# Optimization experiments

Hardware: AMD Instinct MI355X
Metric: run time of the kernel (lower is better)

## Reference

```python
import jax, jax.numpy as jnp
import numpy as np

HIDDEN = 4096
N_HEADS = 32
N_KV_HEADS = 8
HEAD_DIM = 128
ROPE_BASE = 10000.0


def setup_inputs() -> dict:
    key = jax.random.key(0)
    k1, k2, k3, k4, k5 = jax.random.split(key, 5)
    s = 0.02  # init scale for weights
    return {
        "hidden_states": jax.random.normal(k1, (1, 2048, HIDDEN), dtype=jnp.float32),
        "Wq": jax.random.normal(k2, (N_HEADS * HEAD_DIM, HIDDEN), dtype=jnp.float32) * s,
        "Wk": jax.random.normal(k3, (N_KV_HEADS * HEAD_DIM, HIDDEN), dtype=jnp.float32) * s,
        "Wv": jax.random.normal(k4, (N_KV_HEADS * HEAD_DIM, HIDDEN), dtype=jnp.float32) * s,
        "Wo": jax.random.normal(k5, (HIDDEN, HIDDEN), dtype=jnp.float32) * s,
    }


def _rope(x, cos, sin):
    # x: [B, H, T, D]; cos/sin: [T, D/2] -> rotate split halves (Llama style)
    d2 = x.shape[-1] // 2
    x1, x2 = x[..., :d2], x[..., d2:]
    return jnp.concatenate([x1 * cos - x2 * sin, x1 * sin + x2 * cos], axis=-1)


def reference(hidden_states, Wq, Wk, Wv, Wo):
    B, T, _ = hidden_states.shape
    H, Hkv, D = N_HEADS, N_KV_HEADS, HEAD_DIM
    G = H // Hkv  # kv groups

    q = jnp.einsum("bth,qh->btq", hidden_states, Wq).reshape(B, T, H, D).transpose(0, 2, 1, 3)
    k = jnp.einsum("bth,kh->btk", hidden_states, Wk).reshape(B, T, Hkv, D).transpose(0, 2, 1, 3)
    v = jnp.einsum("bth,vh->btv", hidden_states, Wv).reshape(B, T, Hkv, D).transpose(0, 2, 1, 3)

    # RoPE (position_offset = 0)
    positions = jnp.arange(T, dtype=jnp.float32)
    inv_freq = ROPE_BASE ** (-jnp.arange(0, D, 2, dtype=jnp.float32) / D)  # [D/2]
    angles = positions[:, None] * inv_freq[None, :]                        # [T, D/2]
    cos, sin = jnp.cos(angles), jnp.sin(angles)
    q = _rope(q, cos, sin)
    k = _rope(k, cos, sin)

    # GQA attention without materializing expanded K/V: group query heads
    qg = q.reshape(B, Hkv, G, T, D)
    scale = 1.0 / jnp.sqrt(jnp.asarray(D, dtype=q.dtype))
    scores = jnp.einsum("bkgtd,bksd->bkgts", qg, k) * scale  # [B, Hkv, G, T, T]
    causal = jnp.tril(jnp.ones((T, T), dtype=bool))
    scores = jnp.where(causal, scores, jnp.finfo(scores.dtype).min)
    probs = jax.nn.softmax(scores, axis=-1)
    attn = jnp.einsum("bkgts,bksd->bkgtd", probs, v)          # [B, Hkv, G, T, D]
    attn = attn.reshape(B, H, T, D).transpose(0, 2, 1, 3).reshape(B, T, H * D)

    return jnp.einsum("btq,oq->bto", attn, Wo)
```

## Files before the change

kernel.cpp:

```cpp
#include <hip/hip_runtime.h>
#include <stdint.h>

#define T_SEQ   2048
#define HID     4096
#define NH      32
#define NKV     8
#define HD      128
#define QCOLS   6144
#define QK_SCALE 0.08838834764831845f

typedef _Float16 half_t;
typedef _Float16 half8 __attribute__((ext_vector_type(8)));
typedef _Float16 half4v __attribute__((ext_vector_type(4)));
typedef float    f32x4 __attribute__((ext_vector_type(4)));

typedef __attribute__((address_space(1))) const void cg_void;
typedef __attribute__((address_space(3))) void lds_void;

__global__ __launch_bounds__(256) void cast_all_k(const float* __restrict__ X,
                                                  const float* __restrict__ Wq,
                                                  const float* __restrict__ Wk,
                                                  const float* __restrict__ Wv,
                                                  const float* __restrict__ Wo,
                                                  half_t* __restrict__ Xh,
                                                  half_t* __restrict__ Wqkvh,
                                                  half_t* __restrict__ Woh) {
  int i = blockIdx.x * 256 + threadIdx.x;
  const float* src; half_t* dst; int off;
  if (i < 2097152)      { src = X;  dst = Xh;               off = i; }
  else if (i < 6291456) { src = Wq; dst = Wqkvh;            off = i - 2097152; }
  else if (i < 7340032) { src = Wk; dst = Wqkvh + 16777216; off = i - 6291456; }
  else if (i < 8388608) { src = Wv; dst = Wqkvh + 20971520; off = i - 7340032; }
  else                  { src = Wo; dst = Woh;              off = i - 8388608; }
  f32x4 v = *(const f32x4*)(src + (size_t)off * 4);
  half4v o;
  o[0] = (half_t)v[0]; o[1] = (half_t)v[1]; o[2] = (half_t)v[2]; o[3] = (half_t)v[3];
  *(half4v*)(dst + (size_t)off * 4) = o;
}

__global__ __launch_bounds__(256) void rope_tables_k(float* __restrict__ cs) {
  int idx = blockIdx.x * 256 + threadIdx.x;
  int t = idx >> 6, i = idx & 63;
  float inv = expf(-(float)i * 0.14391156831212787f);
  float a = (float)t * inv;
  cs[idx] = cosf(a);
  cs[131072 + idx] = sinf(a);
}

__global__ __launch_bounds__(256) void rope_apply_k(half_t* __restrict__ QKV,
                                                    const float* __restrict__ cs) {
  int idx = blockIdx.x * 256 + threadIdx.x;
  int i = idx & 63;
  int rem = idx >> 6;
  int head = rem % 40;
  int t = rem / 40;
  int colbase = (head < 32) ? head * HD : HID + (head - 32) * HD;
  size_t base = (size_t)t * QCOLS + colbase;
  float c = cs[t * 64 + i], s = cs[131072 + t * 64 + i];
  float x1 = (float)QKV[base + i];
  float x2 = (float)QKV[base + 64 + i];
  float o1 = x1 * c - x2 * s;
  float o2 = x1 * s + x2 * c;
  if (head < 32) { o1 *= QK_SCALE; o2 *= QK_SCALE; }
  QKV[base + i]      = (half_t)o1;
  QKV[base + 64 + i] = (half_t)o2;
}

__global__ __launch_bounds__(256) void transpose_v_k(const half_t* __restrict__ QKV,
                                                     half_t* __restrict__ Vt) {
  int idx = blockIdx.x * 256 + threadIdx.x;
  int d  = idx & 127;
  int ts = (idx >> 7) & 255;
  int kh = idx >> 15;
  half8 o;
#pragma unroll
  for (int i = 0; i < 8; ++i)
    o[i] = QKV[(size_t)(ts * 8 + i) * QCOLS + HID + NKV * HD + kh * HD + d];
  *(half8*)&Vt[(size_t)kh * (HD * T_SEQ) + (size_t)d * T_SEQ + ts * 8] = o;
}

template <int BM, int BN, int OUT_HALF>
__global__ __launch_bounds__(512, 2) void gemm8p_k(const half_t* __restrict__ A,
                                                   const half_t* __restrict__ Bm,
                                                   void* __restrict__ Cout,
                                                   int M, int N, int K) {
  constexpr int MF = BM / 32;
  constexpr int NF = BN / 64;
  constexpr int MH = MF / 2;
  constexpr int LA = BM / 64;
  constexpr int LB = BN / 64;
  __shared__ half_t Al[2][BM * 64];
  __shared__ half_t Bl[2][BN * 64];

  const int nbm = M / BM;
  const int nwg = nbm * (N / BN);
  const int bid = blockIdx.x;
  const int swz = (bid & 7) * (nwg >> 3) + (bid >> 3);
  const int brow = (swz % nbm) * BM;
  const int bcol = (swz / nbm) * BN;
  const int tid = threadIdx.x;
  const int lane = tid & 63, wid = tid >> 6;
  const int wr = wid >> 2, wc = wid & 3;
  const int lr = lane & 15, hi = lane >> 4;
  const int wrow = wr * (MF * 16), wcol = wc * (NF * 16);

  const half_t* Ab = A + (size_t)brow * K;
  const half_t* Bb = Bm + (size_t)bcol * K;

  f32x4 acc[MF][NF] = {};
  half8 afr[MH], bfr[NF];

#define STAGE_A(l, k0, buf) { \
    int c_ = (l) * 512 + tid; int r_ = c_ >> 3, s_ = c_ & 7; \
    __builtin_amdgcn_global_load_lds( \
      (cg_void*)(Ab + (size_t)r_ * K + (k0) + ((s_ ^ (r_ & 7)) * 8)), \
      (lds_void*)(&Al[buf][((l) * 512 + wid * 64) * 8]), 16, 0, 0); }
#define STAGE_B(l, k0, buf) { \
    int c_ = (l) * 512 + tid; int r_ = c_ >> 3, s_ = c_ & 7; \
    __builtin_amdgcn_global_load_lds( \
      (cg_void*)(Bb + (size_t)r_ * K + (k0) + ((s_ ^ (r_ & 7)) * 8)), \
      (lds_void*)(&Bl[buf][((l) * 512 + wid * 64) * 8]), 16, 0, 0); }
#define RD_A(i, mh, kk, buf) { \
    int row_ = wrow + ((mh) * MH + (i)) * 16 + lr; int ks_ = (kk) * 4 + hi; \
    afr[i] = *(const half8*)&Al[buf][row_ * 64 + ((ks_ ^ (row_ & 7)) * 8)]; }
#define RD_B(n, kk, buf) { \
    int row_ = wcol + (n) * 16 + lr; int ks_ = (kk) * 4 + hi; \
    bfr[n] = *(const half8*)&Bl[buf][row_ * 64 + ((ks_ ^ (row_ & 7)) * 8)]; }
#define MFMA_PH(mh) { \
    __builtin_amdgcn_s_setprio(1); \
    _Pragma("unroll") for (int i_ = 0; i_ < MH; ++i_) \
      _Pragma("unroll") for (int n_ = 0; n_ < NF; ++n_) \
        acc[(mh) * MH + i_][n_] = __builtin_amdgcn_mfma_f32_16x16x32_f16( \
            afr[i_], bfr[n_], acc[(mh) * MH + i_][n_], 0, 0, 0); \
    __builtin_amdgcn_s_setprio(0); }

#define DO_TILE(T, BUF) { \
    const int kn_ = ((T) + 1) * 64; const bool pf_ = ((T) + 1) < NT; \
     \
    if (pf_) { _Pragma("unroll") for (int l_ = 0; l_ < LA; ++l_) STAGE_A(l_, kn_, (BUF) ^ 1); } \
    _Pragma("unroll") for (int n_ = 0; n_ < NF; ++n_) RD_B(n_, 0, BUF); \
    _Pragma("unroll") for (int i_ = 0; i_ < MH; ++i_) RD_A(i_, 0, 0, BUF); \
    MFMA_PH(0); \
    __builtin_amdgcn_s_barrier(); __builtin_amdgcn_sched_barrier(0); \
     \
    if (pf_) { _Pragma("unroll") for (int l_ = 0; l_ < LB; ++l_) STAGE_B(l_, kn_, (BUF) ^ 1); } \
    _Pragma("unroll") for (int i_ = 0; i_ < MH; ++i_) RD_A(i_, 1, 0, BUF); \
    MFMA_PH(1); \
    __builtin_amdgcn_s_barrier(); __builtin_amdgcn_sched_barrier(0); \
     \
    _Pragma("unroll") for (int n_ = 0; n_ < NF; ++n_) RD_B(n_, 1, BUF); \
    _Pragma("unroll") for (int i_ = 0; i_ < MH; ++i_) RD_A(i_, 1, 1, BUF); \
    MFMA_PH(1); \
    __builtin_amdgcn_s_barrier(); __builtin_amdgcn_sched_barrier(0); \
     \
    _Pragma("unroll") for (int i_ = 0; i_ < MH; ++i_) RD_A(i_, 0, 1, BUF); \
    MFMA_PH(0); \
    asm volatile("s_waitcnt vmcnt(0)" ::: "memory"); \
    __syncthreads(); }

  const int NT = K / 64;
#pragma unroll
  for (int l_ = 0; l_ < LA; ++l_) STAGE_A(l_, 0, 0);
#pragma unroll
  for (int l_ = 0; l_ < LB; ++l_) STAGE_B(l_, 0, 0);
  asm volatile("s_waitcnt vmcnt(0)" ::: "memory");
  __syncthreads();

  for (int t = 0; t < NT; t += 2) {
    DO_TILE(t, 0);
    DO_TILE(t + 1, 1);
  }

#undef STAGE_A
#undef STAGE_B
#undef RD_A
#undef RD_B
#undef MFMA_PH
#undef DO_TILE

#pragma unroll
  for (int m = 0; m < MF; ++m)
#pragma unroll
    for (int n = 0; n < NF; ++n)
#pragma unroll
      for (int r = 0; r < 4; ++r) {
        int row = brow + wrow + m * 16 + hi * 4 + r;
        int col = bcol + wcol + n * 16 + lr;
        float v = acc[m][n][r];
        if (OUT_HALF) ((half_t*)Cout)[(size_t)row * N + col] = (half_t)v;
        else          ((float*)Cout)[(size_t)row * N + col] = v;
      }
}

__global__ __launch_bounds__(256) void attn_k(const half_t* __restrict__ QKV,
                                              const half_t* __restrict__ Vt,
                                              half_t* __restrict__ Ob) {
  const int bid = blockIdx.x;
  const int qb = 31 - (bid >> 5);
  const int h  = bid & 31;
  const int kh = h >> 2;
  const int tid = threadIdx.x;
  const int lane = tid & 63;
  const int w = tid >> 6;
  const int lr = lane & 15, hi = lane >> 4;
  const int qrow = qb * 64 + w * 16;

  __shared__ half_t Klds[64 * 128];
  __shared__ half_t Vlds[128 * 64];
  __shared__ half_t Plds[4 * 16 * 72];

  const half_t* Qp  = QKV + h * HD;
  const half_t* Kp  = QKV + HID + kh * HD;
  const half_t* Vtp = Vt + (size_t)kh * (HD * T_SEQ);

  half8 qf[4];
#pragma unroll
  for (int kk = 0; kk < 4; ++kk)
    qf[kk] = *(const half8*)&Qp[(size_t)(qrow + lr) * QCOLS + kk * 32 + hi * 8];

  f32x4 acc[8] = {};
  float mrow[4], lrow[4];
#pragma unroll
  for (int r = 0; r < 4; ++r) { mrow[r] = -1e30f; lrow[r] = 0.0f; }

  half_t* Pw = &Plds[w * (16 * 72)];
  const int nt = qb + 1;
  for (int t = 0; t < nt; ++t) {
    const int kv0 = t * 64;
#pragma unroll
    for (int c = 0; c < 4; ++c) {
      int chunk = c * 256 + tid;
      int r = chunk >> 4, s = chunk & 15;
      int cc = (s & 8) | ((s ^ r) & 7);
      __builtin_amdgcn_global_load_lds(
          (cg_void*)(Kp + (size_t)(kv0 + r) * QCOLS + cc * 8),
          (lds_void*)(&Klds[(c * 256 + w * 64) * 8]), 16, 0, 0);
    }
#pragma unroll
    for (int c = 0; c < 4; ++c) {
      int chunk = c * 256 + tid;
      int r = chunk >> 3, s = chunk & 7;
      int cc = (s ^ r) & 7;
      __builtin_amdgcn_global_load_lds(
          (cg_void*)(Vtp + (size_t)r * T_SEQ + kv0 + cc * 8),
          (lds_void*)(&Vlds[(c * 256 + w * 64) * 8]), 16, 0, 0);
    }
    __syncthreads();

    f32x4 s[4] = {};
#pragma unroll
    for (int jt = 0; jt < 4; ++jt)
#pragma unroll
      for (int kk = 0; kk < 4; ++kk) {
        int srow = jt * 16 + lr;
        int sl = kk * 4 + hi;
        int c = (sl & 8) | ((sl ^ srow) & 7);
        half8 kf = *(const half8*)&Klds[srow * 128 + c * 8];
        s[jt] = __builtin_amdgcn_mfma_f32_16x16x32_f16(qf[kk], kf, s[jt], 0, 0, 0);
      }

    if (t == qb) {
#pragma unroll
      for (int jt = 0; jt < 4; ++jt)
#pragma unroll
        for (int r = 0; r < 4; ++r) {
          int ig = qrow + hi * 4 + r;
          int jg = kv0 + jt * 16 + lr;
          if (jg > ig) s[jt][r] = -1e30f;
        }
    }

    float mx[4], scl[4], ls[4];
#pragma unroll
    for (int r = 0; r < 4; ++r)
      mx[r] = fmaxf(fmaxf(s[0][r], s[1][r]), fmaxf(s[2][r], s[3][r]));
#pragma unroll
    for (int off = 1; off < 16; off <<= 1)
#pragma unroll
      for (int r = 0; r < 4; ++r)
        mx[r] = fmaxf(mx[r], __shfl_xor(mx[r], off, 64));
#pragma unroll
    for (int r = 0; r < 4; ++r) {
      float mn = fmaxf(mrow[r], mx[r]);
      scl[r] = __expf(mrow[r] - mn);
      mrow[r] = mn;
      ls[r] = 0.0f;
#pragma unroll
      for (int jt = 0; jt < 4; ++jt) {
        s[jt][r] = __expf(s[jt][r] - mn);
        ls[r] += s[jt][r];
      }
    }
#pragma unroll
    for (int off = 1; off < 16; off <<= 1)
#pragma unroll
      for (int r = 0; r < 4; ++r)
        ls[r] += __shfl_xor(ls[r], off, 64);
#pragma unroll
    for (int r = 0; r < 4; ++r) lrow[r] = lrow[r] * scl[r] + ls[r];
#pragma unroll
    for (int g = 0; g < 8; ++g)
#pragma unroll
      for (int r = 0; r < 4; ++r) acc[g][r] *= scl[r];

#pragma unroll
    for (int jt = 0; jt < 4; ++jt)
#pragma unroll
      for (int r = 0; r < 4; ++r)
        Pw[(hi * 4 + r) * 72 + jt * 16 + lr] = (half_t)s[jt][r];
    half8 pf[2];
#pragma unroll
    for (int jt = 0; jt < 2; ++jt)
      pf[jt] = *(const half8*)&Pw[lr * 72 + jt * 32 + hi * 8];

#pragma unroll
    for (int g = 0; g < 8; ++g)
#pragma unroll
      for (int jt = 0; jt < 2; ++jt) {
        int vrow = g * 16 + lr;
        int sl = jt * 4 + hi;
        int c = (sl ^ vrow) & 7;
        half8 vf = *(const half8*)&Vlds[vrow * 64 + c * 8];
        acc[g] = __builtin_amdgcn_mfma_f32_16x16x32_f16(pf[jt], vf, acc[g], 0, 0, 0);
      }
    __syncthreads();
  }

#pragma unroll
  for (int g = 0; g < 8; ++g)
#pragma unroll
    for (int r = 0; r < 4; ++r) {
      int row = qrow + hi * 4 + r;
      int col = h * HD + g * 16 + lr;
      Ob[(size_t)row * HID + col] = (half_t)(acc[g][r] / lrow[r]);
    }
}

extern "C" void kernel_launch(void* const* d_in, const int* in_sizes, int n_in,
                              void* d_out, int out_size, void* d_ws, size_t ws_size,
                              hipStream_t stream) {
  const float* hs = (const float*)d_in[0];
  const float* Wq = (const float*)d_in[1];
  const float* Wk = (const float*)d_in[2];
  const float* Wv = (const float*)d_in[3];
  const float* Wo = (const float*)d_in[4];
  float* out = (float*)d_out;

  char* ws = (char*)d_ws;
  half_t* Xh    = (half_t*)(ws + 0);
  half_t* Vt    = (half_t*)(ws + 0);
  half_t* Wqkvh = (half_t*)(ws + 16777216);
  half_t* Woh   = (half_t*)(ws + 67108864);
  half_t* QKV   = (half_t*)(ws + 100663296);
  half_t* attnh = (half_t*)(ws + 125829120);
  float*  cs    = (float*)(ws + 142606336);
  if (ws_size < 143654912ull) return;

  cast_all_k<<<49152, 256, 0, stream>>>(hs, Wq, Wk, Wv, Wo, Xh, Wqkvh, Woh);
  rope_tables_k<<<512, 256, 0, stream>>>(cs);

  gemm8p_k<256, 192, 1><<<256, 512, 0, stream>>>(Xh, Wqkvh, (void*)QKV, 2048, 6144, 4096);
  rope_apply_k<<<20480, 256, 0, stream>>>(QKV, cs);
  transpose_v_k<<<1024, 256, 0, stream>>>(QKV, Vt);
  attn_k<<<1024, 256, 0, stream>>>(QKV, Vt, attnh);
  gemm8p_k<128, 256, 0><<<256, 512, 0, stream>>>(attnh, Woh, (void*)out, 2048, 4096, 4096);
}
```

Measured before the change: 336.0 us.

## Deepen GEMM prefetch to two tiles with triple-buffered A and partial vmcnt waits

Replaces the double-buffered, drain-every-tile GEMM main loop with a two-tile-ahead pipeline. A gets three LDS buffers and B keeps two, and B is refilled in place after its last read. Each iteration waits with a partial vmcnt so one tile's global-to-LDS loads stay in flight, instead of a full vmcnt(0) plus syncthreads per tile. This is meant to hide global load latency behind MFMA work, at the cost of more LDS (which may limit occupancy), runtime buffer indices, and subtler synchronisation correctness.

```diff
diff --git a/kernel.cpp b/kernel.cpp
--- a/kernel.cpp
+++ b/kernel.cpp
@@ -89,7 +89,9 @@
   constexpr int MH = MF / 2;
   constexpr int LA = BM / 64;
   constexpr int LB = BN / 64;
-  __shared__ half_t Al[2][BM * 64];
+  constexpr int LA0 = LA / 2, LA1 = LA - LA0;
+  constexpr int VM = LA + LB;
+  __shared__ half_t Al[3][BM * 64];
   __shared__ half_t Bl[2][BN * 64];
 
   const int nbm = M / BM;
@@ -133,42 +135,47 @@
         acc[(mh) * MH + i_][n_] = __builtin_amdgcn_mfma_f32_16x16x32_f16( \
             afr[i_], bfr[n_], acc[(mh) * MH + i_][n_], 0, 0, 0); \
     __builtin_amdgcn_s_setprio(0); }
-
-#define DO_TILE(T, BUF) { \
-    const int kn_ = ((T) + 1) * 64; const bool pf_ = ((T) + 1) < NT; \
-     \
-    if (pf_) { _Pragma("unroll") for (int l_ = 0; l_ < LA; ++l_) STAGE_A(l_, kn_, (BUF) ^ 1); } \
-    _Pragma("unroll") for (int n_ = 0; n_ < NF; ++n_) RD_B(n_, 0, BUF); \
-    _Pragma("unroll") for (int i_ = 0; i_ < MH; ++i_) RD_A(i_, 0, 0, BUF); \
-    MFMA_PH(0); \
-    __builtin_amdgcn_s_barrier(); __builtin_amdgcn_sched_barrier(0); \
-     \
-    if (pf_) { _Pragma("unroll") for (int l_ = 0; l_ < LB; ++l_) STAGE_B(l_, kn_, (BUF) ^ 1); } \
-    _Pragma("unroll") for (int i_ = 0; i_ < MH; ++i_) RD_A(i_, 1, 0, BUF); \
-    MFMA_PH(1); \
-    __builtin_amdgcn_s_barrier(); __builtin_amdgcn_sched_barrier(0); \
-     \
-    _Pragma("unroll") for (int n_ = 0; n_ < NF; ++n_) RD_B(n_, 1, BUF); \
-    _Pragma("unroll") for (int i_ = 0; i_ < MH; ++i_) RD_A(i_, 1, 1, BUF); \
-    MFMA_PH(1); \
-    __builtin_amdgcn_s_barrier(); __builtin_amdgcn_sched_barrier(0); \
-     \
-    _Pragma("unroll") for (int i_ = 0; i_ < MH; ++i_) RD_A(i_, 0, 1, BUF); \
-    MFMA_PH(0); \
-    asm volatile("s_waitcnt vmcnt(0)" ::: "memory"); \
-    __syncthreads(); }
+#define BAR() { __builtin_amdgcn_s_barrier(); __builtin_amdgcn_sched_barrier(0); }
 
   const int NT = K / 64;
 #pragma unroll
   for (int l_ = 0; l_ < LA; ++l_) STAGE_A(l_, 0, 0);
 #pragma unroll
   for (int l_ = 0; l_ < LB; ++l_) STAGE_B(l_, 0, 0);
-  asm volatile("s_waitcnt vmcnt(0)" ::: "memory");
-  __syncthreads();
-
-  for (int t = 0; t < NT; t += 2) {
-    DO_TILE(t, 0);
-    DO_TILE(t + 1, 1);
+#pragma unroll
+  for (int l_ = 0; l_ < LA; ++l_) STAGE_A(l_, 64, 1);
+#pragma unroll
+  for (int l_ = 0; l_ < LB; ++l_) STAGE_B(l_, 64, 1);
+
+  int ab = 0, bb = 0;
+  for (int t = 0; t < NT; ++t) {
+    if (t + 1 < NT) { asm volatile("s_waitcnt vmcnt(%0)" :: "n"(VM) : "memory"); }
+    else            { asm volatile("s_waitcnt vmcnt(0)" ::: "memory"); }
+    BAR();
+
+    int a2 = ab + 2; if (a2 >= 3) a2 -= 3;
+    const bool pf = (t + 2) < NT;
+    const int kn = (t + 2) * 64;
+
+    if (pf) { _Pragma("unroll") for (int l_ = 0; l_ < LA0; ++l_) STAGE_A(l_, kn, a2); }
+    _Pragma("unroll") for (int n_ = 0; n_ < NF; ++n_) RD_B(n_, 0, bb);
+    _Pragma("unroll") for (int i_ = 0; i_ < MH; ++i_) RD_A(i_, 0, 0, ab);
+    MFMA_PH(0);
+    BAR();
+    if (pf) { _Pragma("unroll") for (int l_ = 0; l_ < LA1; ++l_) STAGE_A(LA0 + l_, kn, a2); }
+    _Pragma("unroll") for (int i_ = 0; i_ < MH; ++i_) RD_A(i_, 1, 0, ab);
+    MFMA_PH(1);
+    BAR();
+    _Pragma("unroll") for (int n_ = 0; n_ < NF; ++n_) RD_B(n_, 1, bb);
+    _Pragma("unroll") for (int i_ = 0; i_ < MH; ++i_) RD_A(i_, 1, 1, ab);
+    MFMA_PH(1);
+    BAR();
+    if (pf) { _Pragma("unroll") for (int l_ = 0; l_ < LB; ++l_) STAGE_B(l_, kn, bb); }
+    _Pragma("unroll") for (int i_ = 0; i_ < MH; ++i_) RD_A(i_, 0, 1, ab);
+    MFMA_PH(0);
+
+    ab = (ab + 1 == 3) ? 0 : ab + 1;
+    bb ^= 1;
   }
 
 #undef STAGE_A
@@ -176,7 +183,7 @@
 #undef RD_A
 #undef RD_B
 #undef MFMA_PH
-#undef DO_TILE
+#undef BAR
 
 #pragma unroll
   for (int m = 0; m < MF; ++m)
```

Measured after the change: 397.5 us. 18.3% more time.

## Process two 64-row query subtiles per attention block to reuse K/V tiles

Applied to the files above, without the earlier changes.

Each attention workgroup now handles 128 query rows, split into two 64-row subtiles, instead of 64. Every K/V tile loaded into LDS feeds twice as many MFMAs, which halves the global K/V traffic and the number of barriers per unit of work. The grid shrinks to 512 blocks, with a reordered block-to-query mapping so causal load stays balanced, and launch bounds request 2 blocks per SIMD. The cost is higher register pressure from doubled accumulators and fewer blocks to spread across CUs.

```diff
diff --git a/kernel.cpp b/kernel.cpp
--- a/kernel.cpp
+++ b/kernel.cpp
@@ -192,39 +192,43 @@
       }
 }
 
-__global__ __launch_bounds__(256) void attn_k(const half_t* __restrict__ QKV,
-                                              const half_t* __restrict__ Vt,
-                                              half_t* __restrict__ Ob) {
+__global__ __launch_bounds__(256, 2) void attn_k(const half_t* __restrict__ QKV,
+                                                 const half_t* __restrict__ Vt,
+                                                 half_t* __restrict__ Ob) {
   const int bid = blockIdx.x;
-  const int qb = 31 - (bid >> 5);
+  const int qb = (bid < 256) ? (15 - (bid >> 5)) : ((bid - 256) >> 5);
   const int h  = bid & 31;
   const int kh = h >> 2;
   const int tid = threadIdx.x;
   const int lane = tid & 63;
   const int w = tid >> 6;
   const int lr = lane & 15, hi = lane >> 4;
-  const int qrow = qb * 64 + w * 16;
+  const int qbase = qb * 128;
 
   __shared__ half_t Klds[64 * 128];
   __shared__ half_t Vlds[128 * 64];
-  __shared__ half_t Plds[4 * 16 * 72];
+  __shared__ half_t Plds[4 * 32 * 72];
 
   const half_t* Qp  = QKV + h * HD;
   const half_t* Kp  = QKV + HID + kh * HD;
   const half_t* Vtp = Vt + (size_t)kh * (HD * T_SEQ);
 
-  half8 qf[4];
-#pragma unroll
-  for (int kk = 0; kk < 4; ++kk)
-    qf[kk] = *(const half8*)&Qp[(size_t)(qrow + lr) * QCOLS + kk * 32 + hi * 8];
-
-  f32x4 acc[8] = {};
-  float mrow[4], lrow[4];
-#pragma unroll
-  for (int r = 0; r < 4; ++r) { mrow[r] = -1e30f; lrow[r] = 0.0f; }
-
-  half_t* Pw = &Plds[w * (16 * 72)];
-  const int nt = qb + 1;
+  half8 qf[2][4];
+#pragma unroll
+  for (int s = 0; s < 2; ++s)
+#pragma unroll
+    for (int kk = 0; kk < 4; ++kk)
+      qf[s][kk] = *(const half8*)&Qp[(size_t)(qbase + s * 64 + w * 16 + lr) * QCOLS + kk * 32 + hi * 8];
+
+  f32x4 acc[2][8] = {};
+  float mrow[2][4], lrow[2][4];
+#pragma unroll
+  for (int s = 0; s < 2; ++s)
+#pragma unroll
+    for (int r = 0; r < 4; ++r) { mrow[s][r] = -1e30f; lrow[s][r] = 0.0f; }
+
+  half_t* Pw = &Plds[w * (32 * 72)];
+  const int nt = 2 * qb + 2;
   for (int t = 0; t < nt; ++t) {
     const int kv0 = t * 64;
 #pragma unroll
@@ -247,7 +251,7 @@
     }
     __syncthreads();
 
-    f32x4 s[4] = {};
+    f32x4 sc[2][4] = {};
 #pragma unroll
     for (int jt = 0; jt < 4; ++jt)
 #pragma unroll
@@ -256,62 +260,72 @@
         int sl = kk * 4 + hi;
         int c = (sl & 8) | ((sl ^ srow) & 7);
         half8 kf = *(const half8*)&Klds[srow * 128 + c * 8];
-        s[jt] = __builtin_amdgcn_mfma_f32_16x16x32_f16(qf[kk], kf, s[jt], 0, 0, 0);
-      }
-
-    if (t == qb) {
+        sc[0][jt] = __builtin_amdgcn_mfma_f32_16x16x32_f16(qf[0][kk], kf, sc[0][jt], 0, 0, 0);
+        sc[1][jt] = __builtin_amdgcn_mfma_f32_16x16x32_f16(qf[1][kk], kf, sc[1][jt], 0, 0, 0);
+      }
+
+    if (t >= 2 * qb) {
+#pragma unroll
+      for (int s = 0; s < 2; ++s)
+#pragma unroll
+        for (int jt = 0; jt < 4; ++jt)
+#pragma unroll
+          for (int r = 0; r < 4; ++r) {
+            int ig = qbase + s * 64 + w * 16 + hi * 4 + r;
+            int jg = kv0 + jt * 16 + lr;
+            if (jg > ig) sc[s][jt][r] = -1e30f;
+          }
+    }
+
+#pragma unroll
+    for (int s = 0; s < 2; ++s) {
+      float mx[4], scl[4], ls[4];
+#pragma unroll
+      for (int r = 0; r < 4; ++r)
+        mx[r] = fmaxf(fmaxf(sc[s][0][r], sc[s][1][r]), fmaxf(sc[s][2][r], sc[s][3][r]));
+#pragma unroll
+      for (int off = 1; off < 16; off <<= 1)
+#pragma unroll
+        for (int r = 0; r < 4; ++r)
+          mx[r] = fmaxf(mx[r], __shfl_xor(mx[r], off, 64));
+#pragma unroll
+      for (int r = 0; r < 4; ++r) {
+        float mn = fmaxf(mrow[s][r], mx[r]);
+        scl[r] = __expf(mrow[s][r] - mn);
+        mrow[s][r] = mn;
+        ls[r] = 0.0f;
+#pragma unroll
+        for (int jt = 0; jt < 4; ++jt) {
+          sc[s][jt][r] = __expf(sc[s][jt][r] - mn);
+          ls[r] += sc[s][jt][r];
+        }
+      }
+#pragma unroll
+      for (int off = 1; off < 16; off <<= 1)
+#pragma unroll
+        for (int r = 0; r < 4; ++r)
+          ls[r] += __shfl_xor(ls[r], off, 64);
+#pragma unroll
+      for (int r = 0; r < 4; ++r) lrow[s][r] = lrow[s][r] * scl[r] + ls[r];
+#pragma unroll
+      for (int g = 0; g < 8; ++g)
+#pragma unroll
+        for (int r = 0; r < 4; ++r) acc[s][g][r] *= scl[r];
+    }
+
+#pragma unroll
+    for (int s = 0; s < 2; ++s)
 #pragma unroll
       for (int jt = 0; jt < 4; ++jt)
 #pragma unroll
-        for (int r = 0; r < 4; ++r) {
-          int ig = qrow + hi * 4 + r;
-          int jg = kv0 + jt * 16 + lr;
-          if (jg > ig) s[jt][r] = -1e30f;
-        }
-    }
-
-    float mx[4], scl[4], ls[4];
-#pragma unroll
-    for (int r = 0; r < 4; ++r)
-      mx[r] = fmaxf(fmaxf(s[0][r], s[1][r]), fmaxf(s[2][r], s[3][r]));
-#pragma unroll
-    for (int off = 1; off < 16; off <<= 1)
-#pragma unroll
-      for (int r = 0; r < 4; ++r)
-        mx[r] = fmaxf(mx[r], __shfl_xor(mx[r], off, 64));
-#pragma unroll
-    for (int r = 0; r < 4; ++r) {
-      float mn = fmaxf(mrow[r], mx[r]);
-      scl[r] = __expf(mrow[r] - mn);
-      mrow[r] = mn;
-      ls[r] = 0.0f;
-#pragma unroll
-      for (int jt = 0; jt < 4; ++jt) {
-        s[jt][r] = __expf(s[jt][r] - mn);
-        ls[r] += s[jt][r];
-      }
-    }
-#pragma unroll
-    for (int off = 1; off < 16; off <<= 1)
-#pragma unroll
-      for (int r = 0; r < 4; ++r)
-        ls[r] += __shfl_xor(ls[r], off, 64);
-#pragma unroll
-    for (int r = 0; r < 4; ++r) lrow[r] = lrow[r] * scl[r] + ls[r];
-#pragma unroll
-    for (int g = 0; g < 8; ++g)
-#pragma unroll
-      for (int r = 0; r < 4; ++r) acc[g][r] *= scl[r];
-
-#pragma unroll
-    for (int jt = 0; jt < 4; ++jt)
-#pragma unroll
-      for (int r = 0; r < 4; ++r)
-        Pw[(hi * 4 + r) * 72 + jt * 16 + lr] = (half_t)s[jt][r];
-    half8 pf[2];
-#pragma unroll
-    for (int jt = 0; jt < 2; ++jt)
-      pf[jt] = *(const half8*)&Pw[lr * 72 + jt * 32 + hi * 8];
+        for (int r = 0; r < 4; ++r)
+          Pw[(s * 16 + hi * 4 + r) * 72 + jt * 16 + lr] = (half_t)sc[s][jt][r];
+    half8 pf[2][2];
+#pragma unroll
+    for (int s = 0; s < 2; ++s)
+#pragma unroll
+      for (int jt = 0; jt < 2; ++jt)
+        pf[s][jt] = *(const half8*)&Pw[(s * 16 + lr) * 72 + jt * 32 + hi * 8];
 
 #pragma unroll
     for (int g = 0; g < 8; ++g)
@@ -321,19 +335,22 @@
         int sl = jt * 4 + hi;
         int c = (sl ^ vrow) & 7;
         half8 vf = *(const half8*)&Vlds[vrow * 64 + c * 8];
-        acc[g] = __builtin_amdgcn_mfma_f32_16x16x32_f16(pf[jt], vf, acc[g], 0, 0, 0);
+        acc[0][g] = __builtin_amdgcn_mfma_f32_16x16x32_f16(pf[0][jt], vf, acc[0][g], 0, 0, 0);
+        acc[1][g] = __builtin_amdgcn_mfma_f32_16x16x32_f16(pf[1][jt], vf, acc[1][g], 0, 0, 0);
       }
     __syncthreads();
   }
 
 #pragma unroll
-  for (int g = 0; g < 8; ++g)
-#pragma unroll
-    for (int r = 0; r < 4; ++r) {
-      int row = qrow + hi * 4 + r;
-      int col = h * HD + g * 16 + lr;
-      Ob[(size_t)row * HID + col] = (half_t)(acc[g][r] / lrow[r]);
-    }
+  for (int s = 0; s < 2; ++s)
+#pragma unroll
+    for (int g = 0; g < 8; ++g)
+#pragma unroll
+      for (int r = 0; r < 4; ++r) {
+        int row = qbase + s * 64 + w * 16 + hi * 4 + r;
+        int col = h * HD + g * 16 + lr;
+        Ob[(size_t)row * HID + col] = (half_t)(acc[s][g][r] / lrow[s][r]);
+      }
 }
 
 extern "C" void kernel_launch(void* const* d_in, const int* in_sizes, int n_in,
@@ -362,6 +379,6 @@
   gemm8p_k<256, 192, 1><<<256, 512, 0, stream>>>(Xh, Wqkvh, (void*)QKV, 2048, 6144, 4096);
   rope_apply_k<<<20480, 256, 0, stream>>>(QKV, cs);
   transpose_v_k<<<1024, 256, 0, stream>>>(QKV, Vt);
-  attn_k<<<1024, 256, 0, stream>>>(QKV, Vt, attnh);
+  attn_k<<<512, 256, 0, stream>>>(QKV, Vt, attnh);
   gemm8p_k<128, 256, 0><<<256, 512, 0, stream>>>(attnh, Woh, (void*)out, 2048, 4096, 4096);
 }
```

Result: no change. 336.2 us (+0.0%).

## Double-buffer attention K/V tiles, defer row-sum reduction, merge rope and V transpose

Applied to the files above, without the earlier changes.

The attention kernel now double-buffers K/V tiles in LDS, so the next tile's global-to-LDS load overlaps compute on the current one. It also skips the rescale when no row max grows and moves the cross-lane row-sum reduction to the end, replacing the division with a reciprocal multiply. RoPE application and the V transpose are merged into one launch. The cost is twice the K/V LDS and an occupancy hint that may limit registers.

```diff
diff --git a/kernel.cpp b/kernel.cpp
--- a/kernel.cpp
+++ b/kernel.cpp
@@ -47,36 +47,36 @@
   cs[131072 + idx] = sinf(a);
 }
 
-__global__ __launch_bounds__(256) void rope_apply_k(half_t* __restrict__ QKV,
-                                                    const float* __restrict__ cs) {
-  int idx = blockIdx.x * 256 + threadIdx.x;
-  int i = idx & 63;
-  int rem = idx >> 6;
-  int head = rem % 40;
-  int t = rem / 40;
-  int colbase = (head < 32) ? head * HD : HID + (head - 32) * HD;
-  size_t base = (size_t)t * QCOLS + colbase;
-  float c = cs[t * 64 + i], s = cs[131072 + t * 64 + i];
-  float x1 = (float)QKV[base + i];
-  float x2 = (float)QKV[base + 64 + i];
-  float o1 = x1 * c - x2 * s;
-  float o2 = x1 * s + x2 * c;
-  if (head < 32) { o1 *= QK_SCALE; o2 *= QK_SCALE; }
-  QKV[base + i]      = (half_t)o1;
-  QKV[base + 64 + i] = (half_t)o2;
-}
-
-__global__ __launch_bounds__(256) void transpose_v_k(const half_t* __restrict__ QKV,
-                                                     half_t* __restrict__ Vt) {
-  int idx = blockIdx.x * 256 + threadIdx.x;
-  int d  = idx & 127;
-  int ts = (idx >> 7) & 255;
-  int kh = idx >> 15;
-  half8 o;
-#pragma unroll
-  for (int i = 0; i < 8; ++i)
-    o[i] = QKV[(size_t)(ts * 8 + i) * QCOLS + HID + NKV * HD + kh * HD + d];
-  *(half8*)&Vt[(size_t)kh * (HD * T_SEQ) + (size_t)d * T_SEQ + ts * 8] = o;
+__global__ __launch_bounds__(256) void rope_vt_k(half_t* __restrict__ QKV,
+                                                 const float* __restrict__ cs,
+                                                 half_t* __restrict__ Vt) {
+  if (blockIdx.x < 20480) {
+    int idx = blockIdx.x * 256 + threadIdx.x;
+    int i = idx & 63;
+    int rem = idx >> 6;
+    int head = rem % 40;
+    int t = rem / 40;
+    int colbase = (head < 32) ? head * HD : HID + (head - 32) * HD;
+    size_t base = (size_t)t * QCOLS + colbase;
+    float c = cs[t * 64 + i], s = cs[131072 + t * 64 + i];
+    float x1 = (float)QKV[base + i];
+    float x2 = (float)QKV[base + 64 + i];
+    float o1 = x1 * c - x2 * s;
+    float o2 = x1 * s + x2 * c;
+    if (head < 32) { o1 *= QK_SCALE; o2 *= QK_SCALE; }
+    QKV[base + i]      = (half_t)o1;
+    QKV[base + 64 + i] = (half_t)o2;
+  } else {
+    int idx = (blockIdx.x - 20480) * 256 + threadIdx.x;
+    int d  = idx & 127;
+    int ts = (idx >> 7) & 255;
+    int kh = idx >> 15;
+    half8 o;
+#pragma unroll
+    for (int i = 0; i < 8; ++i)
+      o[i] = QKV[(size_t)(ts * 8 + i) * QCOLS + HID + NKV * HD + kh * HD + d];
+    *(half8*)&Vt[(size_t)kh * (HD * T_SEQ) + (size_t)d * T_SEQ + ts * 8] = o;
+  }
 }
 
 template <int BM, int BN, int OUT_HALF>
@@ -136,23 +136,19 @@
 
 #define DO_TILE(T, BUF) { \
     const int kn_ = ((T) + 1) * 64; const bool pf_ = ((T) + 1) < NT; \
-     \
     if (pf_) { _Pragma("unroll") for (int l_ = 0; l_ < LA; ++l_) STAGE_A(l_, kn_, (BUF) ^ 1); } \
     _Pragma("unroll") for (int n_ = 0; n_ < NF; ++n_) RD_B(n_, 0, BUF); \
     _Pragma("unroll") for (int i_ = 0; i_ < MH; ++i_) RD_A(i_, 0, 0, BUF); \
     MFMA_PH(0); \
     __builtin_amdgcn_s_barrier(); __builtin_amdgcn_sched_barrier(0); \
-     \
     if (pf_) { _Pragma("unroll") for (int l_ = 0; l_ < LB; ++l_) STAGE_B(l_, kn_, (BUF) ^ 1); } \
     _Pragma("unroll") for (int i_ = 0; i_ < MH; ++i_) RD_A(i_, 1, 0, BUF); \
     MFMA_PH(1); \
     __builtin_amdgcn_s_barrier(); __builtin_amdgcn_sched_barrier(0); \
-     \
     _Pragma("unroll") for (int n_ = 0; n_ < NF; ++n_) RD_B(n_, 1, BUF); \
     _Pragma("unroll") for (int i_ = 0; i_ < MH; ++i_) RD_A(i_, 1, 1, BUF); \
     MFMA_PH(1); \
     __builtin_amdgcn_s_barrier(); __builtin_amdgcn_sched_barrier(0); \
-     \
     _Pragma("unroll") for (int i_ = 0; i_ < MH; ++i_) RD_A(i_, 0, 1, BUF); \
     MFMA_PH(0); \
     asm volatile("s_waitcnt vmcnt(0)" ::: "memory"); \
@@ -192,9 +188,9 @@
       }
 }
 
-__global__ __launch_bounds__(256) void attn_k(const half_t* __restrict__ QKV,
-                                              const half_t* __restrict__ Vt,
-                                              half_t* __restrict__ Ob) {
+__global__ __launch_bounds__(256, 2) void attn_k(const half_t* __restrict__ QKV,
+                                                 const half_t* __restrict__ Vt,
+                                                 half_t* __restrict__ Ob) {
   const int bid = blockIdx.x;
   const int qb = 31 - (bid >> 5);
   const int h  = bid & 31;
@@ -205,8 +201,8 @@
   const int lr = lane & 15, hi = lane >> 4;
   const int qrow = qb * 64 + w * 16;
 
-  __shared__ half_t Klds[64 * 128];
-  __shared__ half_t Vlds[128 * 64];
+  __shared__ half_t Klds[2][64 * 128];
+  __shared__ half_t Vlds[2][128 * 64];
   __shared__ half_t Plds[4 * 16 * 72];
 
   const half_t* Qp  = QKV + h * HD;
@@ -224,115 +220,123 @@
   for (int r = 0; r < 4; ++r) { mrow[r] = -1e30f; lrow[r] = 0.0f; }
 
   half_t* Pw = &Plds[w * (16 * 72)];
+
+#define STAGE_KV(kv0, buf) { \
+    _Pragma("unroll") for (int c_ = 0; c_ < 4; ++c_) { \
+      int chunk_ = c_ * 256 + tid; \
+      int r_ = chunk_ >> 4, s_ = chunk_ & 15; \
+      int cc_ = (s_ & 8) | ((s_ ^ r_) & 7); \
+      __builtin_amdgcn_global_load_lds( \
+          (cg_void*)(Kp + (size_t)((kv0) + r_) * QCOLS + cc_ * 8), \
+          (lds_void*)(&Klds[buf][(c_ * 256 + w * 64) * 8]), 16, 0, 0); } \
+    _Pragma("unroll") for (int c_ = 0; c_ < 4; ++c_) { \
+      int chunk_ = c_ * 256 + tid; \
+      int r_ = chunk_ >> 3, s_ = chunk_ & 7; \
+      int cc_ = (s_ ^ r_) & 7; \
+      __builtin_amdgcn_global_load_lds( \
+          (cg_void*)(Vtp + (size_t)r_ * T_SEQ + (kv0) + cc_ * 8), \
+          (lds_void*)(&Vlds[buf][(c_ * 256 + w * 64) * 8]), 16, 0, 0); } }
+
+#define COMPUTE(T, BUF) { \
+    const int kv0_ = (T) * 64; \
+    f32x4 sc[4] = {}; \
+    _Pragma("unroll") for (int jt_ = 0; jt_ < 4; ++jt_) \
+      _Pragma("unroll") for (int kk_ = 0; kk_ < 4; ++kk_) { \
+        int srow_ = jt_ * 16 + lr; \
+        int sl_ = kk_ * 4 + hi; \
+        int c_ = (sl_ & 8) | ((sl_ ^ srow_) & 7); \
+        half8 kf_ = *(const half8*)&Klds[BUF][srow_ * 128 + c_ * 8]; \
+        sc[jt_] = __builtin_amdgcn_mfma_f32_16x16x32_f16(qf[kk_], kf_, sc[jt_], 0, 0, 0); \
+      } \
+    if ((T) == qb) { \
+      _Pragma("unroll") for (int jt_ = 0; jt_ < 4; ++jt_) \
+        _Pragma("unroll") for (int r_ = 0; r_ < 4; ++r_) { \
+          int ig_ = qrow + hi * 4 + r_; \
+          int jg_ = kv0_ + jt_ * 16 + lr; \
+          if (jg_ > ig_) sc[jt_][r_] = -1e30f; \
+        } \
+    } \
+    float mx_[4]; \
+    _Pragma("unroll") for (int r_ = 0; r_ < 4; ++r_) \
+      mx_[r_] = fmaxf(fmaxf(sc[0][r_], sc[1][r_]), fmaxf(sc[2][r_], sc[3][r_])); \
+    _Pragma("unroll") for (int off_ = 1; off_ < 16; off_ <<= 1) \
+      _Pragma("unroll") for (int r_ = 0; r_ < 4; ++r_) \
+        mx_[r_] = fmaxf(mx_[r_], __shfl_xor(mx_[r_], off_, 64)); \
+    bool grow_ = false; \
+    _Pragma("unroll") for (int r_ = 0; r_ < 4; ++r_) grow_ = grow_ || (mx_[r_] > mrow[r_]); \
+    if (__any(grow_)) { \
+      float scl_[4]; \
+      _Pragma("unroll") for (int r_ = 0; r_ < 4; ++r_) { \
+        float mn_ = fmaxf(mrow[r_], mx_[r_]); \
+        scl_[r_] = __expf(mrow[r_] - mn_); \
+        mrow[r_] = mn_; \
+        float ls_ = 0.0f; \
+        _Pragma("unroll") for (int jt_ = 0; jt_ < 4; ++jt_) { \
+          sc[jt_][r_] = __expf(sc[jt_][r_] - mn_); ls_ += sc[jt_][r_]; } \
+        lrow[r_] = lrow[r_] * scl_[r_] + ls_; \
+      } \
+      _Pragma("unroll") for (int g_ = 0; g_ < 8; ++g_) \
+        _Pragma("unroll") for (int r_ = 0; r_ < 4; ++r_) acc[g_][r_] *= scl_[r_]; \
+    } else { \
+      _Pragma("unroll") for (int r_ = 0; r_ < 4; ++r_) { \
+        float ls_ = 0.0f; \
+        _Pragma("unroll") for (int jt_ = 0; jt_ < 4; ++jt_) { \
+          sc[jt_][r_] = __expf(sc[jt_][r_] - mrow[r_]); ls_ += sc[jt_][r_]; } \
+        lrow[r_] += ls_; \
+      } \
+    } \
+    _Pragma("unroll") for (int jt_ = 0; jt_ < 4; ++jt_) \
+      _Pragma("unroll") for (int r_ = 0; r_ < 4; ++r_) \
+        Pw[(hi * 4 + r_) * 72 + jt_ * 16 + lr] = (half_t)sc[jt_][r_]; \
+    half8 pf0_ = *(const half8*)&Pw[lr * 72 + hi * 8]; \
+    half8 pf1_ = *(const half8*)&Pw[lr * 72 + 32 + hi * 8]; \
+    _Pragma("unroll") for (int g_ = 0; g_ < 8; ++g_) { \
+      int vrow_ = g_ * 16 + lr; \
+      { int c0_ = (hi ^ vrow_) & 7; \
+        half8 vf_ = *(const half8*)&Vlds[BUF][vrow_ * 64 + c0_ * 8]; \
+        acc[g_] = __builtin_amdgcn_mfma_f32_16x16x32_f16(pf0_, vf_, acc[g_], 0, 0, 0); } \
+      { int c1_ = ((4 + hi) ^ vrow_) & 7; \
+        half8 vf_ = *(const half8*)&Vlds[BUF][vrow_ * 64 + c1_ * 8]; \
+        acc[g_] = __builtin_amdgcn_mfma_f32_16x16x32_f16(pf1_, vf_, acc[g_], 0, 0, 0); } \
+    } }
+
+#define TILE_SYNC() { asm volatile("s_waitcnt vmcnt(0)" ::: "memory"); \
+                      __builtin_amdgcn_s_barrier(); __builtin_amdgcn_sched_barrier(0); }
+
   const int nt = qb + 1;
-  for (int t = 0; t < nt; ++t) {
-    const int kv0 = t * 64;
-#pragma unroll
-    for (int c = 0; c < 4; ++c) {
-      int chunk = c * 256 + tid;
-      int r = chunk >> 4, s = chunk & 15;
-      int cc = (s & 8) | ((s ^ r) & 7);
-      __builtin_amdgcn_global_load_lds(
-          (cg_void*)(Kp + (size_t)(kv0 + r) * QCOLS + cc * 8),
-          (lds_void*)(&Klds[(c * 256 + w * 64) * 8]), 16, 0, 0);
-    }
-#pragma unroll
-    for (int c = 0; c < 4; ++c) {
-      int chunk = c * 256 + tid;
-      int r = chunk >> 3, s = chunk & 7;
-      int cc = (s ^ r) & 7;
-      __builtin_amdgcn_global_load_lds(
-          (cg_void*)(Vtp + (size_t)r * T_SEQ + kv0 + cc * 8),
-          (lds_void*)(&Vlds[(c * 256 + w * 64) * 8]), 16, 0, 0);
-    }
-    __syncthreads();
-
-    f32x4 s[4] = {};
-#pragma unroll
-    for (int jt = 0; jt < 4; ++jt)
-#pragma unroll
-      for (int kk = 0; kk < 4; ++kk) {
-        int srow = jt * 16 + lr;
-        int sl = kk * 4 + hi;
-        int c = (sl & 8) | ((sl ^ srow) & 7);
-        half8 kf = *(const half8*)&Klds[srow * 128 + c * 8];
-        s[jt] = __builtin_amdgcn_mfma_f32_16x16x32_f16(qf[kk], kf, s[jt], 0, 0, 0);
-      }
-
-    if (t == qb) {
-#pragma unroll
-      for (int jt = 0; jt < 4; ++jt)
-#pragma unroll
-        for (int r = 0; r < 4; ++r) {
-          int ig = qrow + hi * 4 + r;
-          int jg = kv0 + jt * 16 + lr;
-          if (jg > ig) s[jt][r] = -1e30f;
-        }
-    }
-
-    float mx[4], scl[4], ls[4];
-#pragma unroll
-    for (int r = 0; r < 4; ++r)
-      mx[r] = fmaxf(fmaxf(s[0][r], s[1][r]), fmaxf(s[2][r], s[3][r]));
-#pragma unroll
-    for (int off = 1; off < 16; off <<= 1)
-#pragma unroll
-      for (int r = 0; r < 4; ++r)
-        mx[r] = fmaxf(mx[r], __shfl_xor(mx[r], off, 64));
-#pragma unroll
-    for (int r = 0; r < 4; ++r) {
-      float mn = fmaxf(mrow[r], mx[r]);
-      scl[r] = __expf(mrow[r] - mn);
-      mrow[r] = mn;
-      ls[r] = 0.0f;
-#pragma unroll
-      for (int jt = 0; jt < 4; ++jt) {
-        s[jt][r] = __expf(s[jt][r] - mn);
-        ls[r] += s[jt][r];
-      }
-    }
-#pragma unroll
-    for (int off = 1; off < 16; off <<= 1)
-#pragma unroll
-      for (int r = 0; r < 4; ++r)
-        ls[r] += __shfl_xor(ls[r], off, 64);
-#pragma unroll
-    for (int r = 0; r < 4; ++r) lrow[r] = lrow[r] * scl[r] + ls[r];
-#pragma unroll
-    for (int g = 0; g < 8; ++g)
-#pragma unroll
-      for (int r = 0; r < 4; ++r) acc[g][r] *= scl[r];
-
-#pragma unroll
-    for (int jt = 0; jt < 4; ++jt)
-#pragma unroll
-      for (int r = 0; r < 4; ++r)
-        Pw[(hi * 4 + r) * 72 + jt * 16 + lr] = (half_t)s[jt][r];
-    half8 pf[2];
-#pragma unroll
-    for (int jt = 0; jt < 2; ++jt)
-      pf[jt] = *(const half8*)&Pw[lr * 72 + jt * 32 + hi * 8];
-
-#pragma unroll
-    for (int g = 0; g < 8; ++g)
-#pragma unroll
-      for (int jt = 0; jt < 2; ++jt) {
-        int vrow = g * 16 + lr;
-        int sl = jt * 4 + hi;
-        int c = (sl ^ vrow) & 7;
-        half8 vf = *(const half8*)&Vlds[vrow * 64 + c * 8];
-        acc[g] = __builtin_amdgcn_mfma_f32_16x16x32_f16(pf[jt], vf, acc[g], 0, 0, 0);
-      }
-    __syncthreads();
+  STAGE_KV(0, 0);
+  TILE_SYNC();
+
+  int t = 0;
+  for (; t + 2 <= nt; t += 2) {
+    STAGE_KV((t + 1) * 64, 1);
+    COMPUTE(t, 0);
+    TILE_SYNC();
+    if (t + 2 < nt) { STAGE_KV((t + 2) * 64, 0); }
+    COMPUTE(t + 1, 1);
+    TILE_SYNC();
   }
-
+  if (t < nt) { COMPUTE(t, 0); }
+
+#undef STAGE_KV
+#undef COMPUTE
+#undef TILE_SYNC
+
+  float linv[4];
+#pragma unroll
+  for (int r = 0; r < 4; ++r) {
+    float l = lrow[r];
+#pragma unroll
+    for (int off = 1; off < 16; off <<= 1) l += __shfl_xor(l, off, 64);
+    linv[r] = 1.0f / l;
+  }
 #pragma unroll
   for (int g = 0; g < 8; ++g)
 #pragma unroll
     for (int r = 0; r < 4; ++r) {
       int row = qrow + hi * 4 + r;
       int col = h * HD + g * 16 + lr;
-      Ob[(size_t)row * HID + col] = (half_t)(acc[g][r] / lrow[r]);
+      Ob[(size_t)row * HID + col] = (half_t)(acc[g][r] * linv[r]);
     }
 }
 
@@ -360,8 +364,7 @@
   rope_tables_k<<<512, 256, 0, stream>>>(cs);
 
   gemm8p_k<256, 192, 1><<<256, 512, 0, stream>>>(Xh, Wqkvh, (void*)QKV, 2048, 6144, 4096);
-  rope_apply_k<<<20480, 256, 0, stream>>>(QKV, cs);
-  transpose_v_k<<<1024, 256, 0, stream>>>(QKV, Vt);
+  rope_vt_k<<<21504, 256, 0, stream>>>(QKV, cs, Vt);
   attn_k<<<1024, 256, 0, stream>>>(QKV, Vt, attnh);
   gemm8p_k<128, 256, 0><<<256, 512, 0, stream>>>(attnh, Woh, (void*)out, 2048, 4096, 4096);
 }
```

Result: faster. 323.1 us (-3.9%).
